# Optimization experiments

Measured on AMD Instinct MI355X. Metric: run time of the kernel, lower is better.

The kernel has to match this reference:

```python
import jax, jax.numpy as jnp
import numpy as np
import math

DIM = 1024
B, S = 4, 2048

def setup_inputs() -> dict:
    key = jax.random.key(0)
    ks = jax.random.split(key, 7)
    std = 1.0 / math.sqrt(DIM)
    return {
        "hidden_states": jax.random.normal(ks[0], (B, S, DIM), dtype=jnp.float32),
        "W_q": jax.random.uniform(ks[1], (DIM, DIM), jnp.float32, -std, std),
        "b_q": jax.random.uniform(ks[2], (DIM,), jnp.float32, -std, std),
        "W_k": jax.random.uniform(ks[3], (DIM, DIM), jnp.float32, -std, std),
        "b_k": jax.random.uniform(ks[4], (DIM,), jnp.float32, -std, std),
        "W_v": jax.random.uniform(ks[5], (DIM, DIM), jnp.float32, -std, std),
        "b_v": jax.random.uniform(ks[6], (DIM,), jnp.float32, -std, std),
        "scalar": jnp.full((1,), 0.1, dtype=jnp.float32),
    }

def reference(hidden_states, W_q, b_q, W_k, b_k, W_v, b_v, scalar):
    # torch Linear: x @ W.T + b
    Q = hidden_states @ W_q.T + b_q
    K = hidden_states @ W_k.T + b_k
    V = hidden_states @ W_v.T + b_v
    h = DIM // 2
    Q1, Q2 = Q[..., :h], Q[..., h:]
    K1, K2 = K[..., :h], K[..., h:]
    s = 1.0 / math.sqrt(V.shape[-1])  # note: scaled by full dim_model, not half
    A1 = jnp.einsum('bqd,bkd->bqk', Q1, K1) * s
    A2 = jnp.einsum('bqd,bkd->bqk', Q2, K2) * s
    attn = jax.nn.softmax(A1, axis=-1) - scalar * jax.nn.softmax(A2, axis=-1)
    return jnp.einsum('bqk,bkd->bqd', attn, V)
```

## Files before the change

kernel.cpp:

```cpp
#include <hip/hip_runtime.h>

typedef __attribute__((ext_vector_type(8))) __bf16 bf16x8;
typedef __attribute__((ext_vector_type(4))) __bf16 bf16x4;
typedef __attribute__((ext_vector_type(4))) float f32x4;

#define GLD16(gp, lp) __builtin_amdgcn_global_load_lds( \
    (const __attribute__((address_space(1))) void*)(gp), \
    (__attribute__((address_space(3))) void*)(lp), 16, 0, 0)

__global__ __launch_bounds__(256) void cvt_f32_bf16(const float* __restrict__ in,
                                                    __bf16* __restrict__ out, long n) {
  long stride = (long)gridDim.x * 256 * 8;
  for (long i = ((long)blockIdx.x * 256 + threadIdx.x) * 8; i < n; i += stride) {
    float4 a = *(const float4*)(in + i);
    float4 b = *(const float4*)(in + i + 4);
    bf16x8 o;
    o[0] = (__bf16)a.x; o[1] = (__bf16)a.y; o[2] = (__bf16)a.z; o[3] = (__bf16)a.w;
    o[4] = (__bf16)b.x; o[5] = (__bf16)b.y; o[6] = (__bf16)b.z; o[7] = (__bf16)b.w;
    *(bf16x8*)(out + i) = o;
  }
}

__global__ __launch_bounds__(256) void zero_f32(float* __restrict__ p, int n) {
  int i = blockIdx.x * 256 + threadIdx.x;
  if (i < n) p[i] = 0.f;
}

template <int EPI>
__global__ __launch_bounds__(256) void gemm_bt(
    const __bf16* __restrict__ A, const __bf16* __restrict__ BT,
    void* __restrict__ Cv, const float* __restrict__ bias,
    int M, int N, int K,
    long aBatch, long bBatch, long cBatch, int tokPerBatch) {
  __shared__ __bf16 As[128 * 32];
  __shared__ __bf16 Bs[128 * 32];

  const int t = threadIdx.x;
  const int w = t >> 6, l = t & 63;
  const int wr = w >> 1, wc = w & 1;
  const int lr = l & 15, lg = l >> 4;

  const int m0 = blockIdx.y * 128, n0 = blockIdx.x * 128;
  const int z = blockIdx.z;
  const __bf16* Ab = A + (long)z * aBatch + (long)m0 * K;
  const __bf16* Bb = BT + (long)z * bBatch + (long)n0 * K;

  const int srow = t >> 2, scol = (t & 3) * 8;
  const __bf16* ag0 = Ab + (long)srow * K + scol;
  const __bf16* bg0 = Bb + (long)srow * K + scol;
  char* lA = (char*)As + w * 1024;
  char* lB = (char*)Bs + w * 1024;

  f32x4 acc[4][4];
#pragma unroll
  for (int m = 0; m < 4; ++m)
#pragma unroll
    for (int n = 0; n < 4; ++n) acc[m][n] = (f32x4){0.f, 0.f, 0.f, 0.f};

  for (int k0 = 0; k0 < K; k0 += 32) {
    __syncthreads();
    GLD16(ag0 + k0, lA);
    GLD16(ag0 + (long)64 * K + k0, lA + 4096);
    GLD16(bg0 + k0, lB);
    GLD16(bg0 + (long)64 * K + k0, lB + 4096);
    __syncthreads();

    bf16x8 af[4], bf[4];
#pragma unroll
    for (int m = 0; m < 4; ++m)
      af[m] = *(const bf16x8*)&As[(wr * 64 + m * 16 + lr) * 32 + lg * 8];
#pragma unroll
    for (int n = 0; n < 4; ++n)
      bf[n] = *(const bf16x8*)&Bs[(wc * 64 + n * 16 + lr) * 32 + lg * 8];
#pragma unroll
    for (int m = 0; m < 4; ++m)
#pragma unroll
      for (int n = 0; n < 4; ++n)
        acc[m][n] = __builtin_amdgcn_mfma_f32_16x16x32_bf16(af[m], bf[n], acc[m][n], 0, 0, 0);
  }

  if constexpr (EPI == 0) {
    __bf16* C = (__bf16*)Cv + (long)z * cBatch;
#pragma unroll
    for (int m = 0; m < 4; ++m)
#pragma unroll
      for (int n = 0; n < 4; ++n) {
        int colg = n0 + wc * 64 + n * 16 + lr;
        float bv = bias ? bias[colg] : 0.f;
#pragma unroll
        for (int r = 0; r < 4; ++r) {
          int rowg = m0 + wr * 64 + m * 16 + lg * 4 + r;
          C[(long)rowg * N + colg] = (__bf16)(acc[m][n][r] + bv);
        }
      }
  } else if constexpr (EPI == 2) {
    float* C = (float*)Cv + (long)z * cBatch;
#pragma unroll
    for (int m = 0; m < 4; ++m)
#pragma unroll
      for (int n = 0; n < 4; ++n) {
        int colg = n0 + wc * 64 + n * 16 + lr;
#pragma unroll
        for (int r = 0; r < 4; ++r) {
          int rowg = m0 + wr * 64 + m * 16 + lg * 4 + r;
          C[(long)rowg * N + colg] = acc[m][n][r];
        }
      }
  } else {
    __shared__ __bf16 Cs[128 * 136];
#pragma unroll
    for (int m = 0; m < 4; ++m)
#pragma unroll
      for (int n = 0; n < 4; ++n) {
        int cl = wc * 64 + n * 16 + lr;
        float bv = bias ? bias[n0 + cl] : 0.f;
        bf16x4 tmp;
#pragma unroll
        for (int r = 0; r < 4; ++r) tmp[r] = (__bf16)(acc[m][n][r] + bv);
        int rl0 = wr * 64 + m * 16 + lg * 4;
        *(bf16x4*)&Cs[cl * 136 + rl0] = tmp;
      }
    __syncthreads();
    int c = t >> 1, half = t & 1;
    long batch = m0 / tokPerBatch;
    int tok0 = (m0 % tokPerBatch) + half * 64;
    __bf16* C = (__bf16*)Cv + batch * (long)N * tokPerBatch + (long)(n0 + c) * tokPerBatch + tok0;
#pragma unroll
    for (int j = 0; j < 8; ++j)
      *(bf16x8*)(C + j * 8) = *(const bf16x8*)&Cs[c * 136 + half * 64 + j * 8];
  }
}

__global__ __launch_bounds__(256) void qk_gemm(
    const __bf16* __restrict__ Q, const __bf16* __restrict__ Kmat,
    __bf16* __restrict__ E1, __bf16* __restrict__ E2,
    float* __restrict__ sums) {
  __shared__ __bf16 As[128 * 32];
  __shared__ __bf16 Bs[128 * 32];
  __shared__ __bf16 Cs[128 * 136];

  const int t = threadIdx.x;
  const int w = t >> 6, l = t & 63;
  const int wr = w >> 1, wc = w & 1;
  const int lr = l & 15, lg = l >> 4;
  const int z = blockIdx.z, b = z >> 1, h = z & 1;
  const int m0 = blockIdx.y * 128, n0 = blockIdx.x * 128;

  const __bf16* Ab = Q + (long)b * 2048 * 1024 + (long)m0 * 1024 + h * 512;
  const __bf16* Bb = Kmat + (long)b * 2048 * 1024 + (long)n0 * 1024 + h * 512;

  const int srow = t >> 2, scol = (t & 3) * 8;
  const __bf16* ag0 = Ab + (long)srow * 1024 + scol;
  const __bf16* bg0 = Bb + (long)srow * 1024 + scol;
  char* lA = (char*)As + w * 1024;
  char* lB = (char*)Bs + w * 1024;

  f32x4 acc[4][4];
#pragma unroll
  for (int m = 0; m < 4; ++m)
#pragma unroll
    for (int n = 0; n < 4; ++n) acc[m][n] = (f32x4){0.f, 0.f, 0.f, 0.f};

  for (int k0 = 0; k0 < 512; k0 += 32) {
    __syncthreads();
    GLD16(ag0 + k0, lA);
    GLD16(ag0 + (long)64 * 1024 + k0, lA + 4096);
    GLD16(bg0 + k0, lB);
    GLD16(bg0 + (long)64 * 1024 + k0, lB + 4096);
    __syncthreads();

    bf16x8 af[4], bf[4];
#pragma unroll
    for (int m = 0; m < 4; ++m)
      af[m] = *(const bf16x8*)&As[(wr * 64 + m * 16 + lr) * 32 + lg * 8];
#pragma unroll
    for (int n = 0; n < 4; ++n)
      bf[n] = *(const bf16x8*)&Bs[(wc * 64 + n * 16 + lr) * 32 + lg * 8];
#pragma unroll
    for (int m = 0; m < 4; ++m)
#pragma unroll
      for (int n = 0; n < 4; ++n)
        acc[m][n] = __builtin_amdgcn_mfma_f32_16x16x32_bf16(af[m], bf[n], acc[m][n], 0, 0, 0);
  }

  const float s = 0.03125f;
  float ps[4][4];
#pragma unroll
  for (int m = 0; m < 4; ++m)
#pragma unroll
    for (int r = 0; r < 4; ++r) ps[m][r] = 0.f;

#pragma unroll
  for (int m = 0; m < 4; ++m)
#pragma unroll
    for (int n = 0; n < 4; ++n) {
      int cl = wc * 64 + n * 16 + lr;
      int rl0 = wr * 64 + m * 16 + lg * 4;
#pragma unroll
      for (int r = 0; r < 4; ++r) {
        float e = __expf(acc[m][n][r] * s);
        ps[m][r] += e;
        Cs[(rl0 + r) * 136 + cl] = (__bf16)e;
      }
    }

#pragma unroll
  for (int m = 0; m < 4; ++m)
#pragma unroll
    for (int r = 0; r < 4; ++r) {
#pragma unroll
      for (int msk = 1; msk < 16; msk <<= 1)
        ps[m][r] += __shfl_xor(ps[m][r], msk, 64);
    }
  if (lr == 0) {
    float* sb = sums + (long)h * 8192 + (long)b * 2048 + m0 + wr * 64;
#pragma unroll
    for (int m = 0; m < 4; ++m)
#pragma unroll
      for (int r = 0; r < 4; ++r)
        atomicAdd(&sb[m * 16 + lg * 4 + r], ps[m][r]);
  }

  __syncthreads();
  __bf16* EX = h ? E2 : E1;
  int row = t >> 1, half = t & 1;
  __bf16* C = EX + ((long)b * 2048 + m0 + row) * 2048 + n0 + half * 64;
  const __bf16* src = &Cs[row * 136 + half * 64];
#pragma unroll
  for (int j = 0; j < 8; ++j)
    *(bf16x8*)(C + j * 8) = *(const bf16x8*)(src + j * 8);
}

__global__ __launch_bounds__(256) void combine_kernel(
    __bf16* __restrict__ P, const __bf16* __restrict__ E2,
    const float* __restrict__ sums, const float* __restrict__ scalar) {
  const float sc = scalar[0];
  const long total = (long)4 * 2048 * 2048 / 8;
  const long stride = (long)gridDim.x * blockDim.x;
  for (long g = (long)blockIdx.x * blockDim.x + threadIdx.x; g < total; g += stride) {
    long row = g >> 8;
    float rl1 = 1.0f / sums[row];
    float rl2 = sc / sums[8192 + row];
    bf16x8 e1 = *(bf16x8*)(P + g * 8);
    bf16x8 e2 = *(const bf16x8*)(E2 + g * 8);
    bf16x8 o;
#pragma unroll
    for (int i = 0; i < 8; ++i)
      o[i] = (__bf16)((float)e1[i] * rl1 - (float)e2[i] * rl2);
    *(bf16x8*)(P + g * 8) = o;
  }
}

__global__ void diag_kernel(float* out, float v) { out[0] = v; }

extern "C" void kernel_launch(void* const* d_in, const int* in_sizes, int n_in,
                              void* d_out, int out_size, void* d_ws, size_t ws_size,
                              hipStream_t stream) {
  const float* hs = (const float*)d_in[0];
  const float* Wq = (const float*)d_in[1];
  const float* bq = (const float*)d_in[2];
  const float* Wk = (const float*)d_in[3];
  const float* bk = (const float*)d_in[4];
  const float* Wv = (const float*)d_in[5];
  const float* bv = (const float*)d_in[6];
  const float* sc = (const float*)d_in[7];

  const long SZ_QKV = (long)4 * 2048 * 1024;
  const long SZ_E = (long)4 * 2048 * 2048;
  const size_t NEED = (size_t)(SZ_QKV * 2) * 4 + (size_t)(SZ_E * 2) * 2 +
                      (size_t)3 * 1024 * 1024 * 2 + (size_t)4 * 2048 * 2 * 4;
  if (ws_size < NEED) {
    diag_kernel<<<dim3(1), dim3(1), 0, stream>>>((float*)d_out, (float)ws_size);
    return;
  }

  char* ws = (char*)d_ws;
  __bf16* Qb = (__bf16*)ws;   ws += SZ_QKV * 2;
  __bf16* Kb = (__bf16*)ws;   ws += SZ_QKV * 2;
  __bf16* VT = (__bf16*)ws;   ws += SZ_QKV * 2;
  __bf16* E1 = (__bf16*)ws;   ws += SZ_E * 2;
  __bf16* E2 = (__bf16*)ws;   ws += SZ_E * 2;
  __bf16* hsb = (__bf16*)ws;  ws += SZ_QKV * 2;
  __bf16* Wqb = (__bf16*)ws;  ws += (long)1024 * 1024 * 2;
  __bf16* Wkb = (__bf16*)ws;  ws += (long)1024 * 1024 * 2;
  __bf16* Wvb = (__bf16*)ws;  ws += (long)1024 * 1024 * 2;
  float* sums = (float*)ws;

  dim3 blk(256);
  cvt_f32_bf16<<<dim3(2048), blk, 0, stream>>>(hs, hsb, SZ_QKV);
  cvt_f32_bf16<<<dim3(512), blk, 0, stream>>>(Wq, Wqb, (long)1024 * 1024);
  cvt_f32_bf16<<<dim3(512), blk, 0, stream>>>(Wk, Wkb, (long)1024 * 1024);
  cvt_f32_bf16<<<dim3(512), blk, 0, stream>>>(Wv, Wvb, (long)1024 * 1024);
  zero_f32<<<dim3(64), blk, 0, stream>>>(sums, 16384);

  dim3 gProj(8, 64, 1);
  gemm_bt<0><<<gProj, blk, 0, stream>>>(hsb, Wqb, Qb, bq, 8192, 1024, 1024, 0, 0, 0, 2048);
  gemm_bt<0><<<gProj, blk, 0, stream>>>(hsb, Wkb, Kb, bk, 8192, 1024, 1024, 0, 0, 0, 2048);
  gemm_bt<1><<<gProj, blk, 0, stream>>>(hsb, Wvb, VT, bv, 8192, 1024, 1024, 0, 0, 0, 2048);

  qk_gemm<<<dim3(16, 16, 8), blk, 0, stream>>>(Qb, Kb, E1, E2, sums);
  combine_kernel<<<dim3(2048), blk, 0, stream>>>(E1, E2, sums, sc);

  gemm_bt<2><<<dim3(8, 16, 4), blk, 0, stream>>>(E1, VT, d_out, nullptr,
      2048, 1024, 2048, (long)2048 * 2048, (long)1024 * 2048, (long)2048 * 1024, 2048);
}
```

Measured before the change: 363.2 us.

## Fuse softmax combine into PV GEMM and merge Q/K projections

Removes the standalone combine pass. The PV GEMM now loads both exponential matrices, combines them per row with a prescaled factor while staging the A tile in LDS, and applies the 1/sum normalization in the epilogue. The Q and K projections become a single GEMM against concatenated weights, and the weight conversions and sums zeroing merge into one kernel. The hs bf16 buffer also reuses E1 space. This cuts launches and a full read-modify-write of the large attention matrix, but the PV loop now does two global register loads per A element without async LDS loads, which may expose latency.

```diff
diff --git a/kernel.cpp b/kernel.cpp
--- a/kernel.cpp
+++ b/kernel.cpp
@@ -8,30 +8,45 @@
     (const __attribute__((address_space(1))) void*)(gp), \
     (__attribute__((address_space(3))) void*)(lp), 16, 0, 0)
 
+__device__ __forceinline__ void cvt8(const float* __restrict__ in, __bf16* __restrict__ out) {
+  float4 a = *(const float4*)in;
+  float4 b = *(const float4*)(in + 4);
+  bf16x8 o;
+  o[0] = (__bf16)a.x; o[1] = (__bf16)a.y; o[2] = (__bf16)a.z; o[3] = (__bf16)a.w;
+  o[4] = (__bf16)b.x; o[5] = (__bf16)b.y; o[6] = (__bf16)b.z; o[7] = (__bf16)b.w;
+  *(bf16x8*)out = o;
+}
+
 __global__ __launch_bounds__(256) void cvt_f32_bf16(const float* __restrict__ in,
                                                     __bf16* __restrict__ out, long n) {
   long stride = (long)gridDim.x * 256 * 8;
-  for (long i = ((long)blockIdx.x * 256 + threadIdx.x) * 8; i < n; i += stride) {
-    float4 a = *(const float4*)(in + i);
-    float4 b = *(const float4*)(in + i + 4);
-    bf16x8 o;
-    o[0] = (__bf16)a.x; o[1] = (__bf16)a.y; o[2] = (__bf16)a.z; o[3] = (__bf16)a.w;
-    o[4] = (__bf16)b.x; o[5] = (__bf16)b.y; o[6] = (__bf16)b.z; o[7] = (__bf16)b.w;
-    *(bf16x8*)(out + i) = o;
-  }
-}
-
-__global__ __launch_bounds__(256) void zero_f32(float* __restrict__ p, int n) {
-  int i = blockIdx.x * 256 + threadIdx.x;
-  if (i < n) p[i] = 0.f;
+  for (long i = ((long)blockIdx.x * 256 + threadIdx.x) * 8; i < n; i += stride)
+    cvt8(in + i, out + i);
+}
+
+__global__ __launch_bounds__(256) void cvt_weights(
+    const float* __restrict__ Wq, const float* __restrict__ Wk,
+    const float* __restrict__ Wv, const float* __restrict__ bq,
+    const float* __restrict__ bk, __bf16* __restrict__ Wqk,
+    __bf16* __restrict__ Wvb, float* __restrict__ bcat,
+    float* __restrict__ sums) {
+  const long M = 1024 * 1024;
+  long id0 = (long)blockIdx.x * 256 + threadIdx.x;
+  long i = id0 * 8;
+  if (i < M) {
+    cvt8(Wq + i, Wqk + i);
+    cvt8(Wk + i, Wqk + M + i);
+    cvt8(Wv + i, Wvb + i);
+  }
+  if (id0 < 1024) { bcat[id0] = bq[id0]; bcat[1024 + id0] = bk[id0]; }
+  if (id0 < 16384) sums[id0] = 0.f;
 }
 
 template <int EPI>
 __global__ __launch_bounds__(256) void gemm_bt(
     const __bf16* __restrict__ A, const __bf16* __restrict__ BT,
     void* __restrict__ Cv, const float* __restrict__ bias,
-    int M, int N, int K,
-    long aBatch, long bBatch, long cBatch, int tokPerBatch) {
+    int M, int N, int K, int tokPerBatch) {
   __shared__ __bf16 As[128 * 32];
   __shared__ __bf16 Bs[128 * 32];
 
@@ -41,9 +56,8 @@
   const int lr = l & 15, lg = l >> 4;
 
   const int m0 = blockIdx.y * 128, n0 = blockIdx.x * 128;
-  const int z = blockIdx.z;
-  const __bf16* Ab = A + (long)z * aBatch + (long)m0 * K;
-  const __bf16* Bb = BT + (long)z * bBatch + (long)n0 * K;
+  const __bf16* Ab = A + (long)m0 * K;
+  const __bf16* Bb = BT + (long)n0 * K;
 
   const int srow = t >> 2, scol = (t & 3) * 8;
   const __bf16* ag0 = Ab + (long)srow * K + scol;
@@ -80,7 +94,7 @@
   }
 
   if constexpr (EPI == 0) {
-    __bf16* C = (__bf16*)Cv + (long)z * cBatch;
+    __bf16* C = (__bf16*)Cv;
 #pragma unroll
     for (int m = 0; m < 4; ++m)
 #pragma unroll
@@ -93,19 +107,6 @@
           C[(long)rowg * N + colg] = (__bf16)(acc[m][n][r] + bv);
         }
       }
-  } else if constexpr (EPI == 2) {
-    float* C = (float*)Cv + (long)z * cBatch;
-#pragma unroll
-    for (int m = 0; m < 4; ++m)
-#pragma unroll
-      for (int n = 0; n < 4; ++n) {
-        int colg = n0 + wc * 64 + n * 16 + lr;
-#pragma unroll
-        for (int r = 0; r < 4; ++r) {
-          int rowg = m0 + wr * 64 + m * 16 + lg * 4 + r;
-          C[(long)rowg * N + colg] = acc[m][n][r];
-        }
-      }
   } else {
     __shared__ __bf16 Cs[128 * 136];
 #pragma unroll
@@ -132,7 +133,7 @@
 }
 
 __global__ __launch_bounds__(256) void qk_gemm(
-    const __bf16* __restrict__ Q, const __bf16* __restrict__ Kmat,
+    const __bf16* __restrict__ QK,
     __bf16* __restrict__ E1, __bf16* __restrict__ E2,
     float* __restrict__ sums) {
   __shared__ __bf16 As[128 * 32];
@@ -146,12 +147,12 @@
   const int z = blockIdx.z, b = z >> 1, h = z & 1;
   const int m0 = blockIdx.y * 128, n0 = blockIdx.x * 128;
 
-  const __bf16* Ab = Q + (long)b * 2048 * 1024 + (long)m0 * 1024 + h * 512;
-  const __bf16* Bb = Kmat + (long)b * 2048 * 1024 + (long)n0 * 1024 + h * 512;
+  const __bf16* Ab = QK + ((long)b * 2048 + m0) * 2048 + h * 512;
+  const __bf16* Bb = QK + ((long)b * 2048 + n0) * 2048 + 1024 + h * 512;
 
   const int srow = t >> 2, scol = (t & 3) * 8;
-  const __bf16* ag0 = Ab + (long)srow * 1024 + scol;
-  const __bf16* bg0 = Bb + (long)srow * 1024 + scol;
+  const __bf16* ag0 = Ab + (long)srow * 2048 + scol;
+  const __bf16* bg0 = Bb + (long)srow * 2048 + scol;
   char* lA = (char*)As + w * 1024;
   char* lB = (char*)Bs + w * 1024;
 
@@ -164,9 +165,9 @@
   for (int k0 = 0; k0 < 512; k0 += 32) {
     __syncthreads();
     GLD16(ag0 + k0, lA);
-    GLD16(ag0 + (long)64 * 1024 + k0, lA + 4096);
+    GLD16(ag0 + (long)64 * 2048 + k0, lA + 4096);
     GLD16(bg0 + k0, lB);
-    GLD16(bg0 + (long)64 * 1024 + k0, lB + 4096);
+    GLD16(bg0 + (long)64 * 2048 + k0, lB + 4096);
     __syncthreads();
 
     bf16x8 af[4], bf[4];
@@ -231,24 +232,92 @@
     *(bf16x8*)(C + j * 8) = *(const bf16x8*)(src + j * 8);
 }
 
-__global__ __launch_bounds__(256) void combine_kernel(
-    __bf16* __restrict__ P, const __bf16* __restrict__ E2,
+__global__ __launch_bounds__(256) void pv_gemm(
+    const __bf16* __restrict__ E1, const __bf16* __restrict__ E2,
+    const __bf16* __restrict__ VT, float* __restrict__ Out,
     const float* __restrict__ sums, const float* __restrict__ scalar) {
-  const float sc = scalar[0];
-  const long total = (long)4 * 2048 * 2048 / 8;
-  const long stride = (long)gridDim.x * blockDim.x;
-  for (long g = (long)blockIdx.x * blockDim.x + threadIdx.x; g < total; g += stride) {
-    long row = g >> 8;
-    float rl1 = 1.0f / sums[row];
-    float rl2 = sc / sums[8192 + row];
-    bf16x8 e1 = *(bf16x8*)(P + g * 8);
-    bf16x8 e2 = *(const bf16x8*)(E2 + g * 8);
-    bf16x8 o;
-#pragma unroll
-    for (int i = 0; i < 8; ++i)
-      o[i] = (__bf16)((float)e1[i] * rl1 - (float)e2[i] * rl2);
-    *(bf16x8*)(P + g * 8) = o;
-  }
+  __shared__ __bf16 As[128 * 32];
+  __shared__ __bf16 Bs[128 * 32];
+
+  const int t = threadIdx.x;
+  const int w = t >> 6, l = t & 63;
+  const int wr = w >> 1, wc = w & 1;
+  const int lr = l & 15, lg = l >> 4;
+  const int z = blockIdx.z;
+  const int m0 = blockIdx.y * 128, n0 = blockIdx.x * 128;
+
+  const int srow = t >> 2, scol = (t & 3) * 8;
+  const long eOff = (long)z * 2048 * 2048 + (long)m0 * 2048 + (long)srow * 2048 + scol;
+  const __bf16* e1r = E1 + eOff;
+  const __bf16* e2r = E2 + eOff;
+  const long rstep = (long)64 * 2048;
+
+  const float scv = scalar[0];
+  const float* s1 = sums + (long)z * 2048 + m0;
+  const float* s2 = s1 + 8192;
+  const float a0 = scv * s1[srow] / s2[srow];
+  const float a1 = scv * s1[srow + 64] / s2[srow + 64];
+
+  const __bf16* bg0 = VT + (long)z * 1024 * 2048 + ((long)n0 + srow) * 2048 + scol;
+  char* lB = (char*)Bs + w * 1024;
+  __bf16* aw0 = &As[srow * 32 + scol];
+  __bf16* aw1 = &As[(srow + 64) * 32 + scol];
+
+  f32x4 acc[4][4];
+#pragma unroll
+  for (int m = 0; m < 4; ++m)
+#pragma unroll
+    for (int n = 0; n < 4; ++n) acc[m][n] = (f32x4){0.f, 0.f, 0.f, 0.f};
+
+  for (int k0 = 0; k0 < 2048; k0 += 32) {
+    bf16x8 x10 = *(const bf16x8*)(e1r + k0);
+    bf16x8 x20 = *(const bf16x8*)(e2r + k0);
+    bf16x8 x11 = *(const bf16x8*)(e1r + rstep + k0);
+    bf16x8 x21 = *(const bf16x8*)(e2r + rstep + k0);
+    bf16x8 p0, p1;
+#pragma unroll
+    for (int i = 0; i < 8; ++i) {
+      p0[i] = (__bf16)fmaf(-a0, (float)x20[i], (float)x10[i]);
+      p1[i] = (__bf16)fmaf(-a1, (float)x21[i], (float)x11[i]);
+    }
+    __syncthreads();
+    GLD16(bg0 + k0, lB);
+    GLD16(bg0 + (long)64 * 2048 + k0, lB + 4096);
+    *(bf16x8*)aw0 = p0;
+    *(bf16x8*)aw1 = p1;
+    __syncthreads();
+
+    bf16x8 af[4], bf[4];
+#pragma unroll
+    for (int m = 0; m < 4; ++m)
+      af[m] = *(const bf16x8*)&As[(wr * 64 + m * 16 + lr) * 32 + lg * 8];
+#pragma unroll
+    for (int n = 0; n < 4; ++n)
+      bf[n] = *(const bf16x8*)&Bs[(wc * 64 + n * 16 + lr) * 32 + lg * 8];
+#pragma unroll
+    for (int m = 0; m < 4; ++m)
+#pragma unroll
+      for (int n = 0; n < 4; ++n)
+        acc[m][n] = __builtin_amdgcn_mfma_f32_16x16x32_bf16(af[m], bf[n], acc[m][n], 0, 0, 0);
+  }
+
+  float rs[4][4];
+#pragma unroll
+  for (int m = 0; m < 4; ++m)
+#pragma unroll
+    for (int r = 0; r < 4; ++r)
+      rs[m][r] = 1.0f / s1[wr * 64 + m * 16 + lg * 4 + r];
+#pragma unroll
+  for (int m = 0; m < 4; ++m)
+#pragma unroll
+    for (int n = 0; n < 4; ++n) {
+      int colg = n0 + wc * 64 + n * 16 + lr;
+#pragma unroll
+      for (int r = 0; r < 4; ++r) {
+        int rowl = wr * 64 + m * 16 + lg * 4 + r;
+        Out[((long)z * 2048 + m0 + rowl) * 1024 + colg] = acc[m][n][r] * rs[m][r];
+      }
+    }
 }
 
 __global__ void diag_kernel(float* out, float v) { out[0] = v; }
@@ -265,42 +334,36 @@
   const float* bv = (const float*)d_in[6];
   const float* sc = (const float*)d_in[7];
 
-  const long SZ_QKV = (long)4 * 2048 * 1024;
+  const long SZ_HS = (long)4 * 2048 * 1024;
+  const long SZ_QK = (long)8192 * 2048;
   const long SZ_E = (long)4 * 2048 * 2048;
-  const size_t NEED = (size_t)(SZ_QKV * 2) * 4 + (size_t)(SZ_E * 2) * 2 +
-                      (size_t)3 * 1024 * 1024 * 2 + (size_t)4 * 2048 * 2 * 4;
+  const size_t NEED = (size_t)SZ_QK * 2 + (size_t)SZ_HS * 2  +
+                      (size_t)SZ_E * 2 * 2  +
+                      (size_t)(2048 + 1024) * 1024 * 2  +
+                      2048 * 4 + 16384 * 4;
   if (ws_size < NEED) {
     diag_kernel<<<dim3(1), dim3(1), 0, stream>>>((float*)d_out, (float)ws_size);
     return;
   }
 
   char* ws = (char*)d_ws;
-  __bf16* Qb = (__bf16*)ws;   ws += SZ_QKV * 2;
-  __bf16* Kb = (__bf16*)ws;   ws += SZ_QKV * 2;
-  __bf16* VT = (__bf16*)ws;   ws += SZ_QKV * 2;
+  __bf16* QKb = (__bf16*)ws;  ws += SZ_QK * 2;
+  __bf16* VT = (__bf16*)ws;   ws += SZ_HS * 2;
   __bf16* E1 = (__bf16*)ws;   ws += SZ_E * 2;
   __bf16* E2 = (__bf16*)ws;   ws += SZ_E * 2;
-  __bf16* hsb = (__bf16*)ws;  ws += SZ_QKV * 2;
-  __bf16* Wqb = (__bf16*)ws;  ws += (long)1024 * 1024 * 2;
-  __bf16* Wkb = (__bf16*)ws;  ws += (long)1024 * 1024 * 2;
+  __bf16* Wqk = (__bf16*)ws;  ws += (long)2048 * 1024 * 2;
   __bf16* Wvb = (__bf16*)ws;  ws += (long)1024 * 1024 * 2;
+  float* bcat = (float*)ws;   ws += 2048 * 4;
   float* sums = (float*)ws;
+  __bf16* hsb = E1;
 
   dim3 blk(256);
-  cvt_f32_bf16<<<dim3(2048), blk, 0, stream>>>(hs, hsb, SZ_QKV);
-  cvt_f32_bf16<<<dim3(512), blk, 0, stream>>>(Wq, Wqb, (long)1024 * 1024);
-  cvt_f32_bf16<<<dim3(512), blk, 0, stream>>>(Wk, Wkb, (long)1024 * 1024);
-  cvt_f32_bf16<<<dim3(512), blk, 0, stream>>>(Wv, Wvb, (long)1024 * 1024);
-  zero_f32<<<dim3(64), blk, 0, stream>>>(sums, 16384);
-
-  dim3 gProj(8, 64, 1);
-  gemm_bt<0><<<gProj, blk, 0, stream>>>(hsb, Wqb, Qb, bq, 8192, 1024, 1024, 0, 0, 0, 2048);
-  gemm_bt<0><<<gProj, blk, 0, stream>>>(hsb, Wkb, Kb, bk, 8192, 1024, 1024, 0, 0, 0, 2048);
-  gemm_bt<1><<<gProj, blk, 0, stream>>>(hsb, Wvb, VT, bv, 8192, 1024, 1024, 0, 0, 0, 2048);
-
-  qk_gemm<<<dim3(16, 16, 8), blk, 0, stream>>>(Qb, Kb, E1, E2, sums);
-  combine_kernel<<<dim3(2048), blk, 0, stream>>>(E1, E2, sums, sc);
-
-  gemm_bt<2><<<dim3(8, 16, 4), blk, 0, stream>>>(E1, VT, d_out, nullptr,
-      2048, 1024, 2048, (long)2048 * 2048, (long)1024 * 2048, (long)2048 * 1024, 2048);
-}
+  cvt_f32_bf16<<<dim3(2048), blk, 0, stream>>>(hs, hsb, SZ_HS);
+  cvt_weights<<<dim3(512), blk, 0, stream>>>(Wq, Wk, Wv, bq, bk, Wqk, Wvb, bcat, sums);
+
+  gemm_bt<0><<<dim3(16, 64, 1), blk, 0, stream>>>(hsb, Wqk, QKb, bcat, 8192, 2048, 1024, 2048);
+  gemm_bt<1><<<dim3(8, 64, 1), blk, 0, stream>>>(hsb, Wvb, VT, bv, 8192, 1024, 1024, 2048);
+
+  qk_gemm<<<dim3(16, 16, 8), blk, 0, stream>>>(QKb, E1, E2, sums);
+  pv_gemm<<<dim3(8, 16, 4), blk, 0, stream>>>(E1, E2, VT, (float*)d_out, sums, sc);
+}
```

After: 364.3 us. No clear change (+0.3%).
